# Performance work log

Measured on AMD Instinct MI355X. Metric: run time of the kernel, lower is better.

## Reference

```python
import jax, jax.numpy as jnp
import numpy as np

IN_C, OUT_C = 32, 32
M1 = M2 = M3 = 12
CFT_M1 = CFT_M2 = M1 // 4  # 3
L_SEG, M_CHEB = 8, 6


def cft2d(x, m1, m2, L, M):
    # Piecewise Chebyshev projection along H (L segments, M polys), rFFT along W.
    # x: [N, C, H, W] -> complex [N, C, m1, m2]
    N, C, H, W = x.shape
    seg = H // L
    t = jnp.linspace(-1.0, 1.0, seg)
    theta = jnp.arccos(jnp.clip(t, -1.0, 1.0))
    P = jnp.cos(jnp.arange(M)[:, None] * theta[None, :])  # [M, seg] Chebyshev T_k
    xs = x.reshape(N, C, L, seg, W)
    coef = jnp.einsum('nclsw,ms->nclmw', xs, P) / seg      # [N,C,L,M,W]
    coef = coef.reshape(N, C, L * M, W)[:, :, :m1, :]      # keep first m1 coeffs
    return jnp.fft.rfft(coef, axis=-1)[:, :, :, :m2]       # [N,C,m1,m2] complex


def setup_inputs() -> dict:
    key = jax.random.key(0)
    ks = jax.random.split(key, 16)
    B, H, W, D = 4, 64, 64, 64
    scale = 1.0 / (IN_C * OUT_C)
    wshape = (IN_C, OUT_C, M1, M2, M3)
    inp = {'x': jax.random.normal(ks[0], (B, IN_C, H, W, D), dtype=jnp.float32)}
    for i in range(4):
        inp[f'w{i+1}_re'] = scale * jax.random.uniform(ks[1 + 2 * i], wshape, dtype=jnp.float32)
        inp[f'w{i+1}_im'] = scale * jax.random.uniform(ks[2 + 2 * i], wshape, dtype=jnp.float32)
    cft_flat = IN_C * CFT_M1 * CFT_M2 * 2  # 576
    hidden = (IN_C + OUT_C) * 2            # 128
    inp['mlp_w1'] = 0.02 * jax.random.normal(ks[9], (cft_flat, hidden), dtype=jnp.float32)
    inp['mlp_b1'] = jnp.zeros((hidden,), dtype=jnp.float32)
    inp['mlp_w2'] = 0.02 * jax.random.normal(ks[10], (hidden, OUT_C), dtype=jnp.float32)
    inp['mlp_b2'] = jnp.zeros((OUT_C,), dtype=jnp.float32)
    inp['corr_scale'] = jnp.float32(0.1)
    return inp


def reference(x, w1_re, w1_im, w2_re, w2_im, w3_re, w3_im, w4_re, w4_im,
              mlp_w1, mlp_b1, mlp_w2, mlp_b2, corr_scale):
    B, C, H, W, D = x.shape
    O = mlp_w2.shape[1]
    x_ft = jnp.fft.rfftn(x, axes=(-3, -2, -1))  # [B,C,H,W,D//2+1] complex64

    def mix(xb, wre, wim):
        return jnp.einsum('bixyz,ioxyz->boxyz', xb, wre + 1j * wim)

    out_ft = jnp.zeros((B, O, H, W, D // 2 + 1), dtype=x_ft.dtype)
    out_ft = out_ft.at[:, :, :M1, :M2, :M3].set(mix(x_ft[:, :, :M1, :M2, :M3], w1_re, w1_im))
    out_ft = out_ft.at[:, :, -M1:, :M2, :M3].set(mix(x_ft[:, :, -M1:, :M2, :M3], w2_re, w2_im))
    out_ft = out_ft.at[:, :, :M1, -M2:, :M3].set(mix(x_ft[:, :, :M1, -M2:, :M3], w3_re, w3_im))
    out_ft = out_ft.at[:, :, -M1:, -M2:, :M3].set(mix(x_ft[:, :, -M1:, -M2:, :M3], w4_re, w4_im))
    x_fno = jnp.fft.irfftn(out_ft, s=(H, W, D), axes=(-3, -2, -1))

    # Chebyshev-Fourier correction branch over depth slices
    xs = jnp.transpose(x, (0, 4, 1, 2, 3)).reshape(B * D, C, H, W)
    cft = cft2d(xs, CFT_M1, CFT_M2, L_SEG, M_CHEB)                 # [B*D,C,3,3] complex
    cft_flat = jnp.stack([cft.real, cft.imag], axis=-1).reshape(B * D, -1)  # view_as_real order
    h = jax.nn.gelu(cft_flat @ mlp_w1 + mlp_b1, approximate=False)
    corr = h @ mlp_w2 + mlp_b2                                     # [B*D, O]
    corr = jnp.transpose(corr.reshape(B, D, O), (0, 2, 1))[:, :, None, None, :]  # [B,O,1,1,D]
    return x_fno + corr_scale * corr
```

## Files before the change

kernel.cpp:

```cpp
#include <hip/hip_runtime.h>
#include <math.h>


#define CMUL_STEP(t, u) do { float _nx = (t).x*(u).x - (t).y*(u).y; \
    (t).y = (t).x*(u).y + (t).y*(u).x; (t).x = _nx; } while (0)

constexpr float TW_C[64] = {
     1.000000000000000f,  0.995184726672197f,  0.980785280403230f,  0.956940335732209f,
     0.923879532511287f,  0.881921264348355f,  0.831469612302545f,  0.773010453362737f,
     0.707106781186548f,  0.634393284163645f,  0.555570233019602f,  0.471396736825998f,
     0.382683432365090f,  0.290284677254462f,  0.195090322016128f,  0.098017140329561f,
     0.000000000000000f, -0.098017140329561f, -0.195090322016128f, -0.290284677254462f,
    -0.382683432365090f, -0.471396736825998f, -0.555570233019602f, -0.634393284163645f,
    -0.707106781186548f, -0.773010453362737f, -0.831469612302545f, -0.881921264348355f,
    -0.923879532511287f, -0.956940335732209f, -0.980785280403230f, -0.995184726672197f,
    -1.000000000000000f, -0.995184726672197f, -0.980785280403230f, -0.956940335732209f,
    -0.923879532511287f, -0.881921264348355f, -0.831469612302545f, -0.773010453362737f,
    -0.707106781186548f, -0.634393284163645f, -0.555570233019602f, -0.471396736825998f,
    -0.382683432365090f, -0.290284677254462f, -0.195090322016128f, -0.098017140329561f,
     0.000000000000000f,  0.098017140329561f,  0.195090322016128f,  0.290284677254462f,
     0.382683432365090f,  0.471396736825998f,  0.555570233019602f,  0.634393284163645f,
     0.707106781186548f,  0.773010453362737f,  0.831469612302545f,  0.881921264348355f,
     0.923879532511287f,  0.956940335732209f,  0.980785280403230f,  0.995184726672197f
};
constexpr float twc(int m) { return TW_C[m & 63]; }
constexpr float tws(int m) { return TW_C[(m + 48) & 63]; }

static __device__ __forceinline__ void fill_tw(float2* tw, int tid, int nthr) {
    for (int m = tid; m < 64; m += nthr) {
        float s, c;
        sincosf((float)m * 0.09817477042468103f, &s, &c);
        tw[m] = make_float2(c, s);
    }
}

template<int KZ0>
static __device__ __forceinline__ void zstage_wave(const float* __restrict__ xt,
                                                   float2* __restrict__ z1k,
                                                   int w) {
    const float x0v  = xt[w];
    const float x32v = xt[32 * 65 + w];
    float a0x = x0v + (((KZ0    ) & 1) ? -x32v : x32v), a0y = 0.f;
    float a1x = x0v + (((KZ0 + 1) & 1) ? -x32v : x32v), a1y = 0.f;
    float a2x = x0v + (((KZ0 + 2) & 1) ? -x32v : x32v), a2y = 0.f;
    #pragma unroll
    for (int d = 1; d < 32; ++d) {
        const float xa = xt[d * 65 + w];
        const float xb = xt[(64 - d) * 65 + w];
        const float e = xa + xb, o = xa - xb;
        a0x += e * twc((KZ0    ) * d);  a0y -= o * tws((KZ0    ) * d);
        a1x += e * twc((KZ0 + 1) * d);  a1y -= o * tws((KZ0 + 1) * d);
        a2x += e * twc((KZ0 + 2) * d);  a2y -= o * tws((KZ0 + 2) * d);
    }
    z1k[(KZ0    ) * 66 + w] = make_float2(a0x, a0y);
    z1k[(KZ0 + 1) * 66 + w] = make_float2(a1x, a1y);
    z1k[(KZ0 + 2) * 66 + w] = make_float2(a2x, a2y);
}

__global__ __launch_bounds__(256) void k_fwd_zy(const float* __restrict__ x,
                                                float2* __restrict__ X2) {
    __shared__ float xt[64 * 65];
    __shared__ __align__(16) float2 z1k[12 * 66];
    const int tid = threadIdx.x;
    const int blk = blockIdx.x;
    const float4* xrow4 = (const float4*)(x + (size_t)blk * 4096);
    for (int r = 0; r < 4; ++r) {
        int i4 = r * 256 + tid;
        int w = i4 >> 4, d4 = (i4 & 15) << 2;
        float4 v = xrow4[i4];
        xt[(d4 + 0) * 65 + w] = v.x;
        xt[(d4 + 1) * 65 + w] = v.y;
        xt[(d4 + 2) * 65 + w] = v.z;
        xt[(d4 + 3) * 65 + w] = v.w;
    }
    __syncthreads();
    {
        const int q = tid >> 6, w = tid & 63;
        switch (q) {
            case 0: zstage_wave<0>(xt, z1k, w); break;
            case 1: zstage_wave<3>(xt, z1k, w); break;
            case 2: zstage_wave<6>(xt, z1k, w); break;
            default: zstage_wave<9>(xt, z1k, w); break;
        }
    }
    __syncthreads();
    float2* xout = X2 + (size_t)blk * 288;
    if (tid < 156) {
        const int ap = tid / 12, kz = tid - (tid / 12) * 12;
        const float2* zr = &z1k[kz * 66];
        const float2 zw0 = zr[0];
        const float2 zw32 = zr[32];
        const float sg = (ap & 1) ? -1.f : 1.f;
        float2 A  = make_float2(zw0.x + sg * zw32.x, zw0.y + sg * zw32.y);
        float2 Bc = A;
        float s_, c_;
        sincosf((float)ap * 0.09817477042468103f, &s_, &c_);
        const float2 u = make_float2(c_, s_);
        float2 t = u;
        for (int w = 1; w < 32; ++w) {
            float2 za = zr[w];
            float2 zb = zr[64 - w];
            float Ex = za.x + zb.x, Ey = za.y + zb.y;
            float Ox = za.x - zb.x, Oy = za.y - zb.y;
            A.x  += t.x * Ex + t.y * Oy;  A.y  += t.x * Ey - t.y * Ox;
            Bc.x += t.x * Ex - t.y * Oy;  Bc.y += t.x * Ey + t.y * Ox;
            CMUL_STEP(t, u);
        }
        if (ap <= 11) xout[ap * 12 + kz] = A;
        if (ap >= 1)  xout[(24 - ap) * 12 + kz] = Bc;
    }
}

__global__ __launch_bounds__(256) void k_fwd_x(const float2* __restrict__ X2,
                                               float2* __restrict__ X3) {
    __shared__ __align__(16) float2 s2[64 * 12];
    __shared__ float2 tw[64];
    const int tid = threadIdx.x;
    const int blk = blockIdx.x;
    const int ay = blk % 24, bc = blk / 24;
    fill_tw(tw, tid, 256);
    const float2* src = X2 + (size_t)bc * (64 * 288) + ay * 12;
    for (int i4 = tid; i4 < 384; i4 += 256) {
        int hh = i4 / 6, c4 = i4 - hh * 6;
        ((float4*)&s2[hh * 12])[c4] = ((const float4*)(src + (size_t)hh * 288))[c4];
    }
    __syncthreads();
    float2* dst = X3 + (size_t)bc * 6912 + ay * 12;
    if (tid < 156) {
        const int ap = tid / 12, kz = tid - (tid / 12) * 12;
        const float2 zw0 = s2[kz];
        const float2 zw32 = s2[32 * 12 + kz];
        const float sg = (ap & 1) ? -1.f : 1.f;
        float2 A  = make_float2(zw0.x + sg * zw32.x, zw0.y + sg * zw32.y);
        float2 Bc = A;
        const float2 u = tw[ap];
        float2 t = u;
        for (int hh = 1; hh < 32; ++hh) {
            float2 za = s2[hh * 12 + kz];
            float2 zb = s2[(64 - hh) * 12 + kz];
            float Ex = za.x + zb.x, Ey = za.y + zb.y;
            float Ox = za.x - zb.x, Oy = za.y - zb.y;
            A.x  += t.x * Ex + t.y * Oy;  A.y  += t.x * Ey - t.y * Ox;
            Bc.x += t.x * Ex - t.y * Oy;  Bc.y += t.x * Ey + t.y * Ox;
            CMUL_STEP(t, u);
        }
        if (ap <= 11) dst[ap * 288 + kz] = A;
        if (ap >= 1)  dst[(24 - ap) * 288 + kz] = Bc;
    }
}

__global__ __launch_bounds__(384) void k_mix(const float2* __restrict__ X3,
                                             float2* __restrict__ F,
        const float* __restrict__ w1re, const float* __restrict__ w1im,
        const float* __restrict__ w2re, const float* __restrict__ w2im,
        const float* __restrict__ w3re, const float* __restrict__ w3im,
        const float* __restrict__ w4re, const float* __restrict__ w4im) {
    __shared__ float2 xs[128 * 12];
    const int tid = threadIdx.x;
    const int blk = blockIdx.x;
    const int ax = blk / 24, ay = blk % 24;
    const int cx = ax >= 12 ? 1 : 0, cy = ay >= 12 ? 1 : 0;
    const int m1 = ax - cx * 12, m2 = ay - cy * 12;
    const int sel = cx + cy * 2;
    const float* wre = sel == 0 ? w1re : sel == 1 ? w2re : sel == 2 ? w3re : w4re;
    const float* wim = sel == 0 ? w1im : sel == 1 ? w2im : sel == 2 ? w3im : w4im;
    const size_t moff = (size_t)ax * 288 + (size_t)ay * 12;
    for (int i = tid; i < 1536; i += 384) {
        int bi = i / 12, kz = i - bi * 12;
        xs[i] = X3[(size_t)bi * 6912 + moff + kz];
    }
    __syncthreads();
    const int o = tid / 12, kz = tid - (tid / 12) * 12;
    const int wbase = o * 1728 + m1 * 144 + m2 * 12 + kz;
    float2 A0 = make_float2(0.f, 0.f), A1 = A0, A2 = A0, A3 = A0;
    for (int i = 0; i < 32; ++i) {
        float wr = wre[i * 55296 + wbase];
        float wi = wim[i * 55296 + wbase];
        float2 x0 = xs[i * 12 + kz];
        float2 x1 = xs[(32 + i) * 12 + kz];
        float2 x2 = xs[(64 + i) * 12 + kz];
        float2 x3 = xs[(96 + i) * 12 + kz];
        A0.x += x0.x * wr - x0.y * wi; A0.y += x0.x * wi + x0.y * wr;
        A1.x += x1.x * wr - x1.y * wi; A1.y += x1.x * wi + x1.y * wr;
        A2.x += x2.x * wr - x2.y * wi; A2.y += x2.x * wi + x2.y * wr;
        A3.x += x3.x * wr - x3.y * wi; A3.y += x3.x * wi + x3.y * wr;
    }
    F[(size_t)(0 * 32 + o) * 6912 + moff + kz] = A0;
    F[(size_t)(1 * 32 + o) * 6912 + moff + kz] = A1;
    F[(size_t)(2 * 32 + o) * 6912 + moff + kz] = A2;
    F[(size_t)(3 * 32 + o) * 6912 + moff + kz] = A3;
}

__global__ __launch_bounds__(256) void k_inv_x(const float2* __restrict__ F,
                                               float2* __restrict__ Y1) {
    __shared__ __align__(16) float2 fs[24 * 12];
    __shared__ float2 tw[64];
    const int tid = threadIdx.x;
    const int blk = blockIdx.x;
    const int ay = blk % 24, bo = blk / 24;
    fill_tw(tw, tid, 256);
    const float2* src = F + (size_t)bo * 6912 + ay * 12;
    for (int i4 = tid; i4 < 144; i4 += 256) {
        int ax = i4 / 6, c4 = i4 - ax * 6;
        ((float4*)&fs[ax * 12])[c4] = ((const float4*)(src + (size_t)ax * 288))[c4];
    }
    __syncthreads();
    float2* dst = Y1 + (size_t)bo * (64 * 288) + ay * 12;
    for (int idx = tid; idx < 396; idx += 256) {
        int hp = idx / 12, kz = idx - (idx / 12) * 12;
        float2 f0  = fs[kz];
        float2 f12 = fs[12 * 12 + kz];
        float2 t12 = tw[(52 * hp) & 63];
        float2 A, Bc;
        A.x  = f0.x + f12.x * t12.x - f12.y * t12.y;
        A.y  = f0.y + f12.x * t12.y + f12.y * t12.x;
        Bc.x = f0.x + f12.x * t12.x + f12.y * t12.y;
        Bc.y = f0.y + f12.y * t12.x - f12.x * t12.y;
        const float2 u = tw[hp];
        float2 t = u;
        for (int a = 1; a <= 11; ++a) {
            float2 fa = fs[a * 12 + kz];
            float2 fb = fs[(24 - a) * 12 + kz];
            float Ex = fa.x + fb.x, Ey = fa.y + fb.y;
            float Ox = fa.x - fb.x, Oy = fa.y - fb.y;
            A.x  += t.x * Ex - t.y * Oy;  A.y  += t.x * Ey + t.y * Ox;
            Bc.x += t.x * Ex + t.y * Oy;  Bc.y += t.x * Ey - t.y * Ox;
            CMUL_STEP(t, u);
        }
        dst[hp * 288 + kz] = A;
        if (hp >= 1 && hp <= 31) dst[(64 - hp) * 288 + kz] = Bc;
    }
}

__global__ __launch_bounds__(256) void k_cft(const float* __restrict__ x,
                                             float* __restrict__ cft) {
    __shared__ float2 tw[64];
    __shared__ float red[3 * 64 * 18];
    const int tid = threadIdx.x;
    const int blk = blockIdx.x;
    const int d = tid & 63, q = tid >> 6;
    fill_tw(tw, tid, 256);
    __syncthreads();
    float aR[3][3] = {{0.f}}, aI[3][3] = {{0.f}};
    const float* xb = x + (size_t)blk * 262144;
    for (int wi = 0; wi < 16; ++wi) {
        const int w = q * 16 + wi;
        float c0 = 0.f, c1 = 0.f, c2 = 0.f;
        #pragma unroll
        for (int s = 0; s < 8; ++s) {
            float xv = xb[(size_t)(s * 64 + w) * 64 + d];
            float t = (2.0f * (float)s - 7.0f) * (1.0f / 7.0f);
            c0 += xv;
            c1 += xv * t;
            c2 += xv * (2.0f * t * t - 1.0f);
        }
        c0 *= 0.125f; c1 *= 0.125f; c2 *= 0.125f;
        #pragma unroll
        for (int f = 0; f < 3; ++f) {
            float2 t = tw[(f * w) & 63];
            aR[0][f] += c0 * t.x; aI[0][f] -= c0 * t.y;
            aR[1][f] += c1 * t.x; aI[1][f] -= c1 * t.y;
            aR[2][f] += c2 * t.x; aI[2][f] -= c2 * t.y;
        }
    }
    if (q > 0) {
        float* dst = &red[((q - 1) * 64 + d) * 18];
        #pragma unroll
        for (int k = 0; k < 3; ++k)
            #pragma unroll
            for (int f = 0; f < 3; ++f) {
                dst[k * 6 + f * 2]     = aR[k][f];
                dst[k * 6 + f * 2 + 1] = aI[k][f];
            }
    }
    __syncthreads();
    if (q == 0) {
        #pragma unroll
        for (int qq = 0; qq < 3; ++qq) {
            const float* sr = &red[(qq * 64 + d) * 18];
            #pragma unroll
            for (int k = 0; k < 3; ++k)
                #pragma unroll
                for (int f = 0; f < 3; ++f) {
                    aR[k][f] += sr[k * 6 + f * 2];
                    aI[k][f] += sr[k * 6 + f * 2 + 1];
                }
        }
        const int b = blk >> 5, c = blk & 31;
        float* dst = cft + (size_t)(b * 64 + d) * 576 + c * 18;
        #pragma unroll
        for (int k = 0; k < 3; ++k)
            #pragma unroll
            for (int f = 0; f < 3; ++f) {
                dst[k * 6 + f * 2]     = aR[k][f];
                dst[k * 6 + f * 2 + 1] = aI[k][f];
            }
    }
}

__global__ __launch_bounds__(128) void k_mlp(const float* __restrict__ cft,
                                             const float* __restrict__ w1,
                                             const float* __restrict__ b1,
                                             const float* __restrict__ w2,
                                             const float* __restrict__ b2,
                                             const float* __restrict__ cs,
                                             float* __restrict__ corr) {
    __shared__ float row[576];
    __shared__ float hbuf[128];
    const int n = blockIdx.x;
    const int tid = threadIdx.x;
    for (int i = tid; i < 576; i += 128) row[i] = cft[(size_t)n * 576 + i];
    __syncthreads();
    float acc = b1[tid];
    #pragma unroll 8
    for (int k = 0; k < 576; ++k) acc += row[k] * w1[k * 128 + tid];
    hbuf[tid] = 0.5f * acc * (1.0f + erff(acc * 0.70710678118654752f));
    __syncthreads();
    if (tid < 32) {
        float a2 = b2[tid];
        #pragma unroll 8
        for (int k = 0; k < 128; ++k) a2 += hbuf[k] * w2[k * 32 + tid];
        const int b = n >> 6, d = n & 63;
        corr[(b * 32 + tid) * 64 + d] = a2 * cs[0];
    }
}

__global__ __launch_bounds__(256) void k_inv_yz(const float2* __restrict__ Y1,
                                                const float* __restrict__ corr,
                                                float* __restrict__ out) {
    __shared__ __align__(16) float2 y1[288];
    __shared__ __align__(16) float2 y2[64 * 12];
    __shared__ float2 tw[64];
    __shared__ float corrl[64];
    const int tid = threadIdx.x;
    const int blk = blockIdx.x;
    const int bo = blk >> 6;
    fill_tw(tw, tid, 256);
    {
        const float4* src4 = (const float4*)(Y1 + (size_t)blk * 288);
        for (int i4 = tid; i4 < 144; i4 += 256) ((float4*)y1)[i4] = src4[i4];
    }
    if (tid < 64) corrl[tid] = corr[bo * 64 + tid];
    __syncthreads();
    {
        const int w = tid >> 2, kz0 = (tid & 3) * 3;
        float2 a0 = make_float2(0.f, 0.f), a1 = a0, a2 = a0;
        {
            float2 f0 = y1[kz0], f1 = y1[kz0 + 1], f2 = y1[kz0 + 2];
            a0.x += f0.x; a0.y += f0.y;
            a1.x += f1.x; a1.y += f1.y;
            a2.x += f2.x; a2.y += f2.y;
        }
        {
            float2 t = tw[(52 * w) & 63];
            float2 f0 = y1[144 + kz0], f1 = y1[144 + kz0 + 1], f2 = y1[144 + kz0 + 2];
            a0.x += f0.x * t.x - f0.y * t.y; a0.y += f0.x * t.y + f0.y * t.x;
            a1.x += f1.x * t.x - f1.y * t.y; a1.y += f1.x * t.y + f1.y * t.x;
            a2.x += f2.x * t.x - f2.y * t.y; a2.y += f2.x * t.y + f2.y * t.x;
        }
        const float2 u = tw[w];
        float2 t = u;
        for (int a = 1; a <= 11; ++a) {
            const float2* fa = &y1[a * 12 + kz0];
            const float2* fb = &y1[(24 - a) * 12 + kz0];
            float2 p0 = fa[0], p1 = fa[1], p2 = fa[2];
            float2 q0 = fb[0], q1 = fb[1], q2 = fb[2];
            float Ex, Ey, Ox, Oy;
            Ex = p0.x + q0.x; Ey = p0.y + q0.y; Ox = p0.x - q0.x; Oy = p0.y - q0.y;
            a0.x += t.x * Ex - t.y * Oy; a0.y += t.x * Ey + t.y * Ox;
            Ex = p1.x + q1.x; Ey = p1.y + q1.y; Ox = p1.x - q1.x; Oy = p1.y - q1.y;
            a1.x += t.x * Ex - t.y * Oy; a1.y += t.x * Ey + t.y * Ox;
            Ex = p2.x + q2.x; Ey = p2.y + q2.y; Ox = p2.x - q2.x; Oy = p2.y - q2.y;
            a2.x += t.x * Ex - t.y * Oy; a2.y += t.x * Ey + t.y * Ox;
            CMUL_STEP(t, u);
        }
        y2[w * 12 + kz0]     = a0;
        y2[w * 12 + kz0 + 1] = a1;
        y2[w * 12 + kz0 + 2] = a2;
    }
    float ctw[12], stw[12];
    const int d = tid & 63;
    #pragma unroll
    for (int kz = 0; kz < 12; ++kz) {
        float2 t = tw[(kz * d) & 63];
        float sc = (kz == 0 ? 1.0f : 2.0f) * (1.0f / 262144.0f);
        ctw[kz] = t.x * sc;
        stw[kz] = t.y * sc;
    }
    __syncthreads();
    const float cv = corrl[d];
    float* orow = out + (size_t)blk * 4096;
    const int wq = tid >> 6;
    for (int r = 0; r < 16; ++r) {
        int w = r * 4 + wq;
        const float4* yv = (const float4*)&y2[w * 12];
        float4 p0 = yv[0], p1 = yv[1], p2 = yv[2];
        float4 p3 = yv[3], p4 = yv[4], p5 = yv[5];
        float s = cv;
        s += p0.x * ctw[0]  - p0.y * stw[0];
        s += p0.z * ctw[1]  - p0.w * stw[1];
        s += p1.x * ctw[2]  - p1.y * stw[2];
        s += p1.z * ctw[3]  - p1.w * stw[3];
        s += p2.x * ctw[4]  - p2.y * stw[4];
        s += p2.z * ctw[5]  - p2.w * stw[5];
        s += p3.x * ctw[6]  - p3.y * stw[6];
        s += p3.z * ctw[7]  - p3.w * stw[7];
        s += p4.x * ctw[8]  - p4.y * stw[8];
        s += p4.z * ctw[9]  - p4.w * stw[9];
        s += p5.x * ctw[10] - p5.y * stw[10];
        s += p5.z * ctw[11] - p5.w * stw[11];
        orow[w * 64 + d] = s;
    }
}

extern "C" void kernel_launch(void* const* d_in, const int* in_sizes, int n_in,
                              void* d_out, int out_size, void* d_ws, size_t ws_size,
                              hipStream_t stream) {
    const float* x    = (const float*)d_in[0];
    const float* w1re = (const float*)d_in[1];
    const float* w1im = (const float*)d_in[2];
    const float* w2re = (const float*)d_in[3];
    const float* w2im = (const float*)d_in[4];
    const float* w3re = (const float*)d_in[5];
    const float* w3im = (const float*)d_in[6];
    const float* w4re = (const float*)d_in[7];
    const float* w4im = (const float*)d_in[8];
    const float* mw1  = (const float*)d_in[9];
    const float* mb1  = (const float*)d_in[10];
    const float* mw2  = (const float*)d_in[11];
    const float* mb2  = (const float*)d_in[12];
    const float* cs   = (const float*)d_in[13];
    float* out = (float*)d_out;

    char* ws = (char*)d_ws;
    float2* X2   = (float2*)(ws);
    float2* X3   = (float2*)(ws + 18874368);
    float2* F    = (float2*)(ws + 25952256);
    float*  cft  = (float*) (ws + 33030144);
    float*  corr = (float*) (ws + 33619968);
    float2* Y1   = X2;

    hipLaunchKernelGGL(k_fwd_zy, dim3(8192), dim3(256), 0, stream, x, X2);
    hipLaunchKernelGGL(k_fwd_x,  dim3(3072), dim3(256), 0, stream, X2, X3);
    hipLaunchKernelGGL(k_mix,    dim3(576),  dim3(384), 0, stream, X3, F,
                       w1re, w1im, w2re, w2im, w3re, w3im, w4re, w4im);
    hipLaunchKernelGGL(k_inv_x,  dim3(3072), dim3(256), 0, stream, F, Y1);
    hipLaunchKernelGGL(k_cft,    dim3(128),  dim3(256), 0, stream, x, cft);
    hipLaunchKernelGGL(k_mlp,    dim3(256),  dim3(128), 0, stream,
                       cft, mw1, mb1, mw2, mb2, cs, corr);
    hipLaunchKernelGGL(k_inv_yz, dim3(8192), dim3(256), 0, stream, Y1, corr, out);
}
```

Baseline: 468.7 us.

## Store FFT stage inputs row-major and mirrored for vectorized LDS reads

The z-stage of the forward transform now stores each input row contiguously, with a stride of 68, instead of transposing it. Each thread then reads its row with float4 loads from both ends. The z and y/x stages also write a mirrored copy (zB/s2B indexed by 64-w), so the paired-DFT loop in a shared ystage_pair helper reads both operands with aligned float4 loads and a fully unrolled loop. The aim is fewer, wider LDS accesses and fewer scattered single-float transposition stores. The cost is roughly double the shared-memory footprint for the stage buffers and extra store traffic to fill the mirror.

```diff
diff --git a/kernel.cpp b/kernel.cpp
--- a/kernel.cpp
+++ b/kernel.cpp
@@ -34,78 +34,157 @@
     }
 }
 
+static __device__ __forceinline__ void ystage_pair(const float2* __restrict__ Ar,
+                                                   const float2* __restrict__ Br,
+                                                   int ap, float2& A, float2& Bc) {
+    const float2 zw0 = Ar[0];
+    const float2 zw32 = Ar[32];
+    const float sg = (ap & 1) ? -1.f : 1.f;
+    A.x = zw0.x + sg * zw32.x;  A.y = zw0.y + sg * zw32.y;
+    Bc = A;
+    float s_, c_;
+    sincosf((float)ap * 0.09817477042468103f, &s_, &c_);
+    const float2 u = make_float2(c_, s_);
+    float2 t = u;
+    {
+        float2 za = Ar[1], zb = Br[1];
+        float Ex = za.x + zb.x, Ey = za.y + zb.y;
+        float Ox = za.x - zb.x, Oy = za.y - zb.y;
+        A.x  += t.x * Ex + t.y * Oy;  A.y  += t.x * Ey - t.y * Ox;
+        Bc.x += t.x * Ex - t.y * Oy;  Bc.y += t.x * Ey + t.y * Ox;
+    }
+    #pragma unroll
+    for (int w = 2; w < 32; w += 2) {
+        CMUL_STEP(t, u);
+        const float4 a4 = *(const float4*)(Ar + w);
+        const float4 b4 = *(const float4*)(Br + w);
+        {
+            float Ex = a4.x + b4.x, Ey = a4.y + b4.y;
+            float Ox = a4.x - b4.x, Oy = a4.y - b4.y;
+            A.x  += t.x * Ex + t.y * Oy;  A.y  += t.x * Ey - t.y * Ox;
+            Bc.x += t.x * Ex - t.y * Oy;  Bc.y += t.x * Ey + t.y * Ox;
+        }
+        CMUL_STEP(t, u);
+        {
+            float Ex = a4.z + b4.z, Ey = a4.w + b4.w;
+            float Ox = a4.z - b4.z, Oy = a4.w - b4.w;
+            A.x  += t.x * Ex + t.y * Oy;  A.y  += t.x * Ey - t.y * Ox;
+            Bc.x += t.x * Ex - t.y * Oy;  Bc.y += t.x * Ey + t.y * Ox;
+        }
+    }
+}
+
 template<int KZ0>
-static __device__ __forceinline__ void zstage_wave(const float* __restrict__ xt,
-                                                   float2* __restrict__ z1k,
+static __device__ __forceinline__ void zstage_wave(const float* __restrict__ row,
+                                                   float2* __restrict__ zA,
+                                                   float2* __restrict__ zB,
                                                    int w) {
-    const float x0v  = xt[w];
-    const float x32v = xt[32 * 65 + w];
-    float a0x = x0v + (((KZ0    ) & 1) ? -x32v : x32v), a0y = 0.f;
-    float a1x = x0v + (((KZ0 + 1) & 1) ? -x32v : x32v), a1y = 0.f;
-    float a2x = x0v + (((KZ0 + 2) & 1) ? -x32v : x32v), a2y = 0.f;
-    #pragma unroll
-    for (int d = 1; d < 32; ++d) {
-        const float xa = xt[d * 65 + w];
-        const float xb = xt[(64 - d) * 65 + w];
-        const float e = xa + xb, o = xa - xb;
-        a0x += e * twc((KZ0    ) * d);  a0y -= o * tws((KZ0    ) * d);
-        a1x += e * twc((KZ0 + 1) * d);  a1y -= o * tws((KZ0 + 1) * d);
-        a2x += e * twc((KZ0 + 2) * d);  a2y -= o * tws((KZ0 + 2) * d);
-    }
-    z1k[(KZ0    ) * 66 + w] = make_float2(a0x, a0y);
-    z1k[(KZ0 + 1) * 66 + w] = make_float2(a1x, a1y);
-    z1k[(KZ0 + 2) * 66 + w] = make_float2(a2x, a2y);
+    float a0x, a0y = 0.f, a1x, a1y = 0.f, a2x, a2y = 0.f;
+#define ACCD(dd, xa, xb) do { \
+    const float e_ = (xa) + (xb), o_ = (xa) - (xb); \
+    a0x += e_ * twc((KZ0    ) * (dd));  a0y -= o_ * tws((KZ0    ) * (dd)); \
+    a1x += e_ * twc((KZ0 + 1) * (dd));  a1y -= o_ * tws((KZ0 + 1) * (dd)); \
+    a2x += e_ * twc((KZ0 + 2) * (dd));  a2y -= o_ * tws((KZ0 + 2) * (dd)); } while (0)
+    float4 qa  = *(const float4*)(row + 0);
+    float4 qm1 = *(const float4*)(row + 60);
+    float4 qm0 = *(const float4*)(row + 56);
+    const float x0v = qa.x;
+    a0x = x0v; a1x = x0v; a2x = x0v;
+    ACCD(1, qa.y, qm1.w);
+    ACCD(2, qa.z, qm1.z);
+    ACCD(3, qa.w, qm1.y);
+    float mnext = qm1.x;
+    qa = *(const float4*)(row + 4);
+    ACCD(4, qa.x, mnext);
+    ACCD(5, qa.y, qm0.w);
+    ACCD(6, qa.z, qm0.z);
+    ACCD(7, qa.w, qm0.y);
+    mnext = qm0.x;
+    qm0 = *(const float4*)(row + 52);
+    qa  = *(const float4*)(row + 8);
+    ACCD(8,  qa.x, mnext);
+    ACCD(9,  qa.y, qm0.w);
+    ACCD(10, qa.z, qm0.z);
+    ACCD(11, qa.w, qm0.y);
+    mnext = qm0.x;
+    qm0 = *(const float4*)(row + 48);
+    qa  = *(const float4*)(row + 12);
+    ACCD(12, qa.x, mnext);
+    ACCD(13, qa.y, qm0.w);
+    ACCD(14, qa.z, qm0.z);
+    ACCD(15, qa.w, qm0.y);
+    mnext = qm0.x;
+    qm0 = *(const float4*)(row + 44);
+    qa  = *(const float4*)(row + 16);
+    ACCD(16, qa.x, mnext);
+    ACCD(17, qa.y, qm0.w);
+    ACCD(18, qa.z, qm0.z);
+    ACCD(19, qa.w, qm0.y);
+    mnext = qm0.x;
+    qm0 = *(const float4*)(row + 40);
+    qa  = *(const float4*)(row + 20);
+    ACCD(20, qa.x, mnext);
+    ACCD(21, qa.y, qm0.w);
+    ACCD(22, qa.z, qm0.z);
+    ACCD(23, qa.w, qm0.y);
+    mnext = qm0.x;
+    qm0 = *(const float4*)(row + 36);
+    qa  = *(const float4*)(row + 24);
+    ACCD(24, qa.x, mnext);
+    ACCD(25, qa.y, qm0.w);
+    ACCD(26, qa.z, qm0.z);
+    ACCD(27, qa.w, qm0.y);
+    mnext = qm0.x;
+    qm0 = *(const float4*)(row + 32);
+    qa  = *(const float4*)(row + 28);
+    ACCD(28, qa.x, mnext);
+    ACCD(29, qa.y, qm0.w);
+    ACCD(30, qa.z, qm0.z);
+    ACCD(31, qa.w, qm0.y);
+    const float x32v = qm0.x;
+#undef ACCD
+    const float s0 = ((KZ0     & 1)) ? -x32v : x32v;
+    const float s1 = (((KZ0+1) & 1)) ? -x32v : x32v;
+    a0x += s0; a1x += s1; a2x += s0;
+    zA[(KZ0    ) * 66 + w] = make_float2(a0x, a0y);
+    zA[(KZ0 + 1) * 66 + w] = make_float2(a1x, a1y);
+    zA[(KZ0 + 2) * 66 + w] = make_float2(a2x, a2y);
+    const int wm = 64 - w;
+    zB[(KZ0    ) * 66 + wm] = make_float2(a0x, a0y);
+    zB[(KZ0 + 1) * 66 + wm] = make_float2(a1x, a1y);
+    zB[(KZ0 + 2) * 66 + wm] = make_float2(a2x, a2y);
 }
 
 __global__ __launch_bounds__(256) void k_fwd_zy(const float* __restrict__ x,
                                                 float2* __restrict__ X2) {
-    __shared__ float xt[64 * 65];
-    __shared__ __align__(16) float2 z1k[12 * 66];
+    __shared__ __align__(16) float xt[64 * 68];
+    __shared__ __align__(16) float2 zA[12 * 66];
+    __shared__ __align__(16) float2 zB[12 * 66];
     const int tid = threadIdx.x;
     const int blk = blockIdx.x;
     const float4* xrow4 = (const float4*)(x + (size_t)blk * 4096);
     for (int r = 0; r < 4; ++r) {
         int i4 = r * 256 + tid;
         int w = i4 >> 4, d4 = (i4 & 15) << 2;
-        float4 v = xrow4[i4];
-        xt[(d4 + 0) * 65 + w] = v.x;
-        xt[(d4 + 1) * 65 + w] = v.y;
-        xt[(d4 + 2) * 65 + w] = v.z;
-        xt[(d4 + 3) * 65 + w] = v.w;
+        *(float4*)&xt[w * 68 + d4] = xrow4[i4];
     }
     __syncthreads();
     {
         const int q = tid >> 6, w = tid & 63;
+        const float* row = &xt[w * 68];
         switch (q) {
-            case 0: zstage_wave<0>(xt, z1k, w); break;
-            case 1: zstage_wave<3>(xt, z1k, w); break;
-            case 2: zstage_wave<6>(xt, z1k, w); break;
-            default: zstage_wave<9>(xt, z1k, w); break;
+            case 0: zstage_wave<0>(row, zA, zB, w); break;
+            case 1: zstage_wave<3>(row, zA, zB, w); break;
+            case 2: zstage_wave<6>(row, zA, zB, w); break;
+            default: zstage_wave<9>(row, zA, zB, w); break;
         }
     }
     __syncthreads();
     float2* xout = X2 + (size_t)blk * 288;
     if (tid < 156) {
         const int ap = tid / 12, kz = tid - (tid / 12) * 12;
-        const float2* zr = &z1k[kz * 66];
-        const float2 zw0 = zr[0];
-        const float2 zw32 = zr[32];
-        const float sg = (ap & 1) ? -1.f : 1.f;
-        float2 A  = make_float2(zw0.x + sg * zw32.x, zw0.y + sg * zw32.y);
-        float2 Bc = A;
-        float s_, c_;
-        sincosf((float)ap * 0.09817477042468103f, &s_, &c_);
-        const float2 u = make_float2(c_, s_);
-        float2 t = u;
-        for (int w = 1; w < 32; ++w) {
-            float2 za = zr[w];
-            float2 zb = zr[64 - w];
-            float Ex = za.x + zb.x, Ey = za.y + zb.y;
-            float Ox = za.x - zb.x, Oy = za.y - zb.y;
-            A.x  += t.x * Ex + t.y * Oy;  A.y  += t.x * Ey - t.y * Ox;
-            Bc.x += t.x * Ex - t.y * Oy;  Bc.y += t.x * Ey + t.y * Ox;
-            CMUL_STEP(t, u);
-        }
+        float2 A, Bc;
+        ystage_pair(&zA[kz * 66], &zB[kz * 66], ap, A, Bc);
         if (ap <= 11) xout[ap * 12 + kz] = A;
         if (ap >= 1)  xout[(24 - ap) * 12 + kz] = Bc;
     }
@@ -113,37 +192,27 @@
 
 __global__ __launch_bounds__(256) void k_fwd_x(const float2* __restrict__ X2,
                                                float2* __restrict__ X3) {
-    __shared__ __align__(16) float2 s2[64 * 12];
-    __shared__ float2 tw[64];
+    __shared__ __align__(16) float2 s2A[12 * 66];
+    __shared__ __align__(16) float2 s2B[12 * 66];
     const int tid = threadIdx.x;
     const int blk = blockIdx.x;
     const int ay = blk % 24, bc = blk / 24;
-    fill_tw(tw, tid, 256);
     const float2* src = X2 + (size_t)bc * (64 * 288) + ay * 12;
     for (int i4 = tid; i4 < 384; i4 += 256) {
         int hh = i4 / 6, c4 = i4 - hh * 6;
-        ((float4*)&s2[hh * 12])[c4] = ((const float4*)(src + (size_t)hh * 288))[c4];
+        float4 v = ((const float4*)(src + (size_t)hh * 288))[c4];
+        int kz = 2 * c4;
+        s2A[kz * 66 + hh]            = make_float2(v.x, v.y);
+        s2A[(kz + 1) * 66 + hh]      = make_float2(v.z, v.w);
+        s2B[kz * 66 + (64 - hh)]     = make_float2(v.x, v.y);
+        s2B[(kz + 1) * 66 + (64 - hh)] = make_float2(v.z, v.w);
     }
     __syncthreads();
     float2* dst = X3 + (size_t)bc * 6912 + ay * 12;
     if (tid < 156) {
         const int ap = tid / 12, kz = tid - (tid / 12) * 12;
-        const float2 zw0 = s2[kz];
-        const float2 zw32 = s2[32 * 12 + kz];
-        const float sg = (ap & 1) ? -1.f : 1.f;
-        float2 A  = make_float2(zw0.x + sg * zw32.x, zw0.y + sg * zw32.y);
-        float2 Bc = A;
-        const float2 u = tw[ap];
-        float2 t = u;
-        for (int hh = 1; hh < 32; ++hh) {
-            float2 za = s2[hh * 12 + kz];
-            float2 zb = s2[(64 - hh) * 12 + kz];
-            float Ex = za.x + zb.x, Ey = za.y + zb.y;
-            float Ox = za.x - zb.x, Oy = za.y - zb.y;
-            A.x  += t.x * Ex + t.y * Oy;  A.y  += t.x * Ey - t.y * Ox;
-            Bc.x += t.x * Ex - t.y * Oy;  Bc.y += t.x * Ey + t.y * Ox;
-            CMUL_STEP(t, u);
-        }
+        float2 A, Bc;
+        ystage_pair(&s2A[kz * 66], &s2B[kz * 66], ap, A, Bc);
         if (ap <= 11) dst[ap * 288 + kz] = A;
         if (ap >= 1)  dst[(24 - ap) * 288 + kz] = Bc;
     }
```

New measurement: 479.7 us. +2.3%, slower.
